# Kernel optimization log

Measured on AMD Instinct MI355X. Metric: run time of the kernel, lower is better.

## Reference

```python
import jax, jax.numpy as jnp
import numpy as np

N_HEADS = 8
N_GROUPS = 8  # n_channels=256 > 64
COLOR_WEIGHT = 1.2
EPS = 1e-5


def setup_inputs() -> dict:
    key = jax.random.key(0)
    ks = jax.random.split(key, 6)
    B, C, H, W = 16, 256, 32, 32
    x = jax.random.normal(ks[0], (B, C, H, W), dtype=jnp.float32)
    std = 0.02
    wq = jax.random.normal(ks[1], (C, C), dtype=jnp.float32) * std
    wk = jax.random.normal(ks[2], (C, C), dtype=jnp.float32) * std
    wv = jax.random.normal(ks[3], (C, C), dtype=jnp.float32) * std
    wo = jax.random.normal(ks[4], (C, C), dtype=jnp.float32) * std
    bq = jnp.zeros((C,), jnp.float32)
    bk = jnp.zeros((C,), jnp.float32)
    bv = jnp.zeros((C,), jnp.float32)
    bo = jnp.zeros((C,), jnp.float32)
    gn_w = jnp.ones((C,), jnp.float32)
    gn_b = jnp.zeros((C,), jnp.float32)
    return {"x": x, "wq": wq, "bq": bq, "wk": wk, "bk": bk,
            "wv": wv, "bv": bv, "wo": wo, "bo": bo,
            "gn_w": gn_w, "gn_b": gn_b}


def reference(x, wq, bq, wk, bk, wv, bv, wo, bo, gn_w, gn_b):
    B, C, H, W = x.shape
    S = H * W
    nh = N_HEADS
    hd = C // nh
    scale = hd ** (-0.5)

    # GroupNorm over (channels_per_group, spatial) per sample
    xf = x.reshape(B, C, S)
    xg = xf.reshape(B, N_GROUPS, (C // N_GROUPS) * S)
    mean = xg.mean(axis=-1, keepdims=True)
    var = xg.var(axis=-1, keepdims=True)
    xn = ((xg - mean) * jax.lax.rsqrt(var + EPS)).reshape(B, C, S)
    xn = xn * gn_w[None, :, None] + gn_b[None, :, None]

    xt = jnp.swapaxes(xn, 1, 2)  # [B, S, C]
    q = xt @ wq.T + bq
    k = xt @ wk.T + bk
    v = xt @ wv.T + bv
    # [B, S, C] -> [B, nh, S, hd]
    q = q.reshape(B, S, nh, hd).transpose(0, 2, 1, 3)
    k = k.reshape(B, S, nh, hd).transpose(0, 2, 1, 3)
    v = v.reshape(B, S, nh, hd).transpose(0, 2, 1, 3)

    attn = jnp.einsum('bhid,bhjd->bhij', q, k) * scale  # [B, nh, S, S]
    # color bias (is_grayscale=False path): k.transpose(-2,-1).reshape(B,nh,S,hd)
    k_color = jnp.swapaxes(k, -2, -1).reshape(B, nh, S, hd)
    color_attn = jnp.abs(q - k_color).mean(axis=-1, keepdims=True)  # [B,nh,S,1]
    attn = attn + COLOR_WEIGHT * color_attn
    attn = jax.nn.softmax(attn, axis=-1)
    # dropout is inference no-op

    out = jnp.einsum('bhij,bhjd->bhid', attn, v)  # [B, nh, S, hd]
    out = out.transpose(0, 2, 1, 3).reshape(B, S, C)
    out = out @ wo.T + bo
    out = jnp.swapaxes(out, 1, 2).reshape(B, C, H, W)
    return out
```

## Files before the change

kernel.cpp:

```cpp
#include <hip/hip_runtime.h>


typedef __attribute__((ext_vector_type(8))) short bf16x8;
typedef __attribute__((ext_vector_type(4))) float f32x4;

static __device__ __forceinline__ unsigned cvt_pk(float lo, float hi) {
  unsigned r;
  asm("v_cvt_pk_bf16_f32 %0, %1, %2" : "=v"(r) : "v"(lo), "v"(hi));
  return r;
}

__global__ __launch_bounds__(256) void gn_stats(
    const float* __restrict__ x, float2* __restrict__ stats) {
  __shared__ float red[8];
  int bg = blockIdx.x;
  const float4* x4 = (const float4*)(x + (size_t)bg * 32 * 1024);
  int tid = threadIdx.x;
  float s = 0.f, ss = 0.f;
  for (int i = tid; i < 8192; i += 256) {
    float4 vv = x4[i];
    s += (vv.x + vv.y) + (vv.z + vv.w);
    ss += vv.x * vv.x + vv.y * vv.y + vv.z * vv.z + vv.w * vv.w;
  }
#pragma unroll
  for (int o = 32; o > 0; o >>= 1) {
    s += __shfl_down(s, o);
    ss += __shfl_down(ss, o);
  }
  if ((tid & 63) == 0) { red[tid >> 6] = s; red[4 + (tid >> 6)] = ss; }
  __syncthreads();
  if (tid == 0) {
    float S = (red[0] + red[1]) + (red[2] + red[3]);
    float SS = (red[4] + red[5]) + (red[6] + red[7]);
    float mean = S * (1.f / 32768.f);
    float var = SS * (1.f / 32768.f) - mean * mean;
    stats[bg] = make_float2(mean, rsqrtf(var + 1e-5f));
  }
}

__global__ __launch_bounds__(256) void wconv(
    const float* __restrict__ w0, const float* __restrict__ w1,
    const float* __restrict__ w2, const float* __restrict__ w3,
    short* __restrict__ o0, short* __restrict__ o1,
    short* __restrict__ o2, short* __restrict__ o3) {
  int sel = blockIdx.y;
  const float* src = sel == 0 ? w0 : sel == 1 ? w1 : sel == 2 ? w2 : w3;
  short* dst = sel == 0 ? o0 : sel == 1 ? o1 : sel == 2 ? o2 : o3;
  int i = (blockIdx.x * 256 + threadIdx.x) * 8;
  float4 a = *(const float4*)(src + i);
  float4 b = *(const float4*)(src + i + 4);
  uint4 r;
  r.x = cvt_pk(a.x, a.y);
  r.y = cvt_pk(a.z, a.w);
  r.z = cvt_pk(b.x, b.y);
  r.w = cvt_pk(b.z, b.w);
  *(uint4*)(dst + i) = r;
}

__global__ __launch_bounds__(256, 4) void qkv_mfma(
    const float* __restrict__ x, const float2* __restrict__ stats,
    const float* __restrict__ gnw, const float* __restrict__ gnb,
    const short* __restrict__ Wq, const short* __restrict__ Wk,
    const short* __restrict__ Wv,
    const float* __restrict__ bq, const float* __restrict__ bk,
    const float* __restrict__ bv, short* __restrict__ outq,
    short* __restrict__ outk, short* __restrict__ outvt, float scaleq) {
  __shared__ __align__(16) char smem[20480];
  short* As = (short*)smem;
  int tid = threadIdx.x;
  int m0 = blockIdx.x * 64, n0 = blockIdx.y * 64;
  int w = tid >> 6, lane = tid & 63, g = lane >> 4, c = lane & 15;
  int wm = w >> 1, wn = w & 1;
  int srow = tid >> 2, sk = (tid & 3) * 8;
  int bsmp = m0 >> 10, s0 = m0 & 1023;
  int c2 = tid & 15, sg = tid >> 4;
  const float4* xb = (const float4*)(x + (size_t)(bsmp * 256) * 1024);
  unsigned* A32 = (unsigned*)As;
  f32x4 accq[2][2], acck[2][2], accv[2][2];
#pragma unroll
  for (int i = 0; i < 2; ++i)
#pragma unroll
    for (int j = 0; j < 2; ++j) {
      accq[i][j] = (f32x4){0.f, 0.f, 0.f, 0.f};
      acck[i][j] = (f32x4){0.f, 0.f, 0.f, 0.f};
      accv[i][j] = (f32x4){0.f, 0.f, 0.f, 0.f};
    }
  for (int kb = 0; kb < 8; ++kb) {
    float2 st = stats[bsmp * 8 + kb];
    int ch0 = kb * 32 + c2 * 2;
    float a0 = gnw[ch0] * st.y, b0v = gnb[ch0] - st.x * a0;
    float a1 = gnw[ch0 + 1] * st.y, b1v = gnb[ch0 + 1] - st.x * a1;
    float4 u = xb[(size_t)ch0 * 256 + (s0 >> 2) + sg];
    float4 v = xb[(size_t)(ch0 + 1) * 256 + (s0 >> 2) + sg];
    __syncthreads();
    {
      int r0 = (sg * 4) * 20 + c2;
      A32[r0]      = cvt_pk(u.x * a0 + b0v, v.x * a1 + b1v);
      A32[r0 + 20] = cvt_pk(u.y * a0 + b0v, v.y * a1 + b1v);
      A32[r0 + 40] = cvt_pk(u.z * a0 + b0v, v.z * a1 + b1v);
      A32[r0 + 60] = cvt_pk(u.w * a0 + b0v, v.w * a1 + b1v);
    }
    *(bf16x8*)(As + 2560 + srow * 40 + sk) =
        *(const bf16x8*)(Wq + (size_t)(n0 + srow) * 256 + kb * 32 + sk);
    *(bf16x8*)(As + 5120 + srow * 40 + sk) =
        *(const bf16x8*)(Wk + (size_t)(n0 + srow) * 256 + kb * 32 + sk);
    *(bf16x8*)(As + 7680 + srow * 40 + sk) =
        *(const bf16x8*)(Wv + (size_t)(n0 + srow) * 256 + kb * 32 + sk);
    __syncthreads();
    bf16x8 af[2], wfq[2], wfk[2], wfv[2];
#pragma unroll
    for (int i = 0; i < 2; ++i)
      af[i] = *(const bf16x8*)(As + (wm * 32 + i * 16 + c) * 40 + g * 8);
#pragma unroll
    for (int j = 0; j < 2; ++j) {
      int rr = (wn * 32 + j * 16 + c) * 40 + g * 8;
      wfq[j] = *(const bf16x8*)(As + 2560 + rr);
      wfk[j] = *(const bf16x8*)(As + 5120 + rr);
      wfv[j] = *(const bf16x8*)(As + 7680 + rr);
    }
#pragma unroll
    for (int i = 0; i < 2; ++i)
#pragma unroll
      for (int j = 0; j < 2; ++j) {
        accq[i][j] = __builtin_amdgcn_mfma_f32_16x16x32_bf16(wfq[j], af[i], accq[i][j], 0, 0, 0);
        acck[i][j] = __builtin_amdgcn_mfma_f32_16x16x32_bf16(wfk[j], af[i], acck[i][j], 0, 0, 0);
        accv[i][j] = __builtin_amdgcn_mfma_f32_16x16x32_bf16(af[i], wfv[j], accv[i][j], 0, 0, 0);
      }
  }
  __syncthreads();
  short* Tb = (short*)smem;
  int mrd = tid >> 2, ncol = (tid & 3) * 16;
#pragma unroll
  for (int i = 0; i < 2; ++i)
#pragma unroll
    for (int j = 0; j < 2; ++j) {
      float4 b4 = *(const float4*)&bq[n0 + wn * 32 + j * 16 + 4 * g];
      float v0 = (accq[i][j][0] + b4.x) * scaleq;
      float v1 = (accq[i][j][1] + b4.y) * scaleq;
      float v2 = (accq[i][j][2] + b4.z) * scaleq;
      float v3 = (accq[i][j][3] + b4.w) * scaleq;
      *(uint2*)(Tb + (wm * 32 + i * 16 + c) * 72 + wn * 32 + j * 16 + 4 * g) =
          make_uint2(cvt_pk(v0, v1), cvt_pk(v2, v3));
    }
  __syncthreads();
  {
    bf16x8 r0 = *(const bf16x8*)(Tb + mrd * 72 + ncol);
    bf16x8 r1 = *(const bf16x8*)(Tb + mrd * 72 + ncol + 8);
    short* dst = outq + (size_t)(m0 + mrd) * 256 + n0 + ncol;
    *(bf16x8*)dst = r0;
    *(bf16x8*)(dst + 8) = r1;
  }
  __syncthreads();
#pragma unroll
  for (int i = 0; i < 2; ++i)
#pragma unroll
    for (int j = 0; j < 2; ++j) {
      float4 b4 = *(const float4*)&bk[n0 + wn * 32 + j * 16 + 4 * g];
      float v0 = acck[i][j][0] + b4.x;
      float v1 = acck[i][j][1] + b4.y;
      float v2 = acck[i][j][2] + b4.z;
      float v3 = acck[i][j][3] + b4.w;
      *(uint2*)(Tb + (wm * 32 + i * 16 + c) * 72 + wn * 32 + j * 16 + 4 * g) =
          make_uint2(cvt_pk(v0, v1), cvt_pk(v2, v3));
    }
  __syncthreads();
  {
    bf16x8 r0 = *(const bf16x8*)(Tb + mrd * 72 + ncol);
    bf16x8 r1 = *(const bf16x8*)(Tb + mrd * 72 + ncol + 8);
    short* dst = outk + (size_t)(m0 + mrd) * 256 + n0 + ncol;
    *(bf16x8*)dst = r0;
    *(bf16x8*)(dst + 8) = r1;
  }
  __syncthreads();
#pragma unroll
  for (int i = 0; i < 2; ++i)
#pragma unroll
    for (int j = 0; j < 2; ++j) {
      float bvv = bv[n0 + wn * 32 + j * 16 + c];
      float v0 = accv[i][j][0] + bvv;
      float v1 = accv[i][j][1] + bvv;
      float v2 = accv[i][j][2] + bvv;
      float v3 = accv[i][j][3] + bvv;
      *(uint2*)(Tb + (wn * 32 + j * 16 + c) * 72 + wm * 32 + i * 16 + 4 * g) =
          make_uint2(cvt_pk(v0, v1), cvt_pk(v2, v3));
    }
  __syncthreads();
  {
    bf16x8 r0 = *(const bf16x8*)(Tb + mrd * 72 + ncol);
    bf16x8 r1 = *(const bf16x8*)(Tb + mrd * 72 + ncol + 8);
    short* dst = outvt + (size_t)(bsmp * 256 + n0 + mrd) * 1024 + s0 + ncol;
    *(bf16x8*)dst = r0;
    *(bf16x8*)(dst + 8) = r1;
  }
}

#define KSTR 40
#define VSTR 72
#define PSTR 72

__global__ __launch_bounds__(256, 4) void flash_mfma(
    const short* __restrict__ q, const short* __restrict__ k,
    const short* __restrict__ vt, short* __restrict__ out) {
  __shared__ short Ks[2][64 * KSTR];
  __shared__ short Vts[2][32 * VSTR];
  __shared__ short Ps[4 * 32 * PSTR];
  int bh = blockIdx.x, qt = blockIdx.y;
  int b = bh >> 3, h = bh & 7;
  int tid = threadIdx.x;
  int w = tid >> 6, lane = tid & 63, g = lane >> 4, c = lane & 15;
  short* Psw = Ps + w * 32 * PSTR;
  const size_t qrow0 = (size_t)b * 1024 + qt * 128 + w * 32;
  const int hoff = h * 32;
  bf16x8 aq[2];
#pragma unroll
  for (int mt = 0; mt < 2; ++mt)
    aq[mt] = *(const bf16x8*)(q + (qrow0 + mt * 16 + c) * 256 + hoff + g * 8);
  bf16x8 ones;
#pragma unroll
  for (int i = 0; i < 8; ++i) ones[i] = (short)0x3F80;
  f32x4 o_acc[2][2], accl[2];
#pragma unroll
  for (int mt = 0; mt < 2; ++mt) {
    accl[mt] = (f32x4){0.f, 0.f, 0.f, 0.f};
#pragma unroll
    for (int nt = 0; nt < 2; ++nt) o_acc[mt][nt] = (f32x4){0.f, 0.f, 0.f, 0.f};
  }
  const int kr = tid >> 2, kch = (tid & 3) * 8;
  const int vr = tid >> 3, vch = (tid & 7) * 8;
  const short* kbase = k + ((size_t)b * 1024) * 256 + hoff;
  const short* vbase = vt + (((size_t)b * 8 + h) * 32) * 1024;
  {
    bf16x8 k0 = *(const bf16x8*)(kbase + (size_t)kr * 256 + kch);
    bf16x8 v0 = *(const bf16x8*)(vbase + (size_t)vr * 1024 + vch);
    *(bf16x8*)(&Ks[0][kr * KSTR + kch]) = k0;
    *(bf16x8*)(&Vts[0][vr * VSTR + vch]) = v0;
  }
  __syncthreads();
  int cur = 0;
#pragma unroll 2
  for (int t = 0; t < 16; ++t) {
    bf16x8 kN, vN;
    if (t < 15) {
      kN = *(const bf16x8*)(kbase + (size_t)((t + 1) * 64 + kr) * 256 + kch);
      vN = *(const bf16x8*)(vbase + (size_t)vr * 1024 + (t + 1) * 64 + vch);
    }
    bf16x8 bk4[4];
#pragma unroll
    for (int kt = 0; kt < 4; ++kt)
      bk4[kt] = *(const bf16x8*)(&Ks[cur][(kt * 16 + c) * KSTR + g * 8]);
    f32x4 sc[2][4];
#pragma unroll
    for (int mt = 0; mt < 2; ++mt)
#pragma unroll
      for (int kt = 0; kt < 4; ++kt)
        sc[mt][kt] = __builtin_amdgcn_mfma_f32_16x16x32_bf16(
            bk4[kt], aq[mt], (f32x4){0.f, 0.f, 0.f, 0.f}, 0, 0, 0);
#pragma unroll
    for (int mt = 0; mt < 2; ++mt)
#pragma unroll
      for (int kt = 0; kt < 4; ++kt) {
        float p0 = __builtin_amdgcn_exp2f(sc[mt][kt][0]);
        float p1 = __builtin_amdgcn_exp2f(sc[mt][kt][1]);
        float p2 = __builtin_amdgcn_exp2f(sc[mt][kt][2]);
        float p3 = __builtin_amdgcn_exp2f(sc[mt][kt][3]);
        *(uint2*)(Psw + (mt * 16 + c) * PSTR + kt * 16 + 4 * g) =
            make_uint2(cvt_pk(p0, p1), cvt_pk(p2, p3));
      }
#pragma unroll
    for (int jt = 0; jt < 2; ++jt) {
      bf16x8 av[2], bp[2];
#pragma unroll
      for (int nt = 0; nt < 2; ++nt)
        av[nt] = *(const bf16x8*)(&Vts[cur][(nt * 16 + c) * VSTR + jt * 32 + g * 8]);
#pragma unroll
      for (int mt = 0; mt < 2; ++mt)
        bp[mt] = *(const bf16x8*)(Psw + (mt * 16 + c) * PSTR + jt * 32 + g * 8);
#pragma unroll
      for (int mt = 0; mt < 2; ++mt) {
#pragma unroll
        for (int nt = 0; nt < 2; ++nt)
          o_acc[mt][nt] = __builtin_amdgcn_mfma_f32_16x16x32_bf16(
              av[nt], bp[mt], o_acc[mt][nt], 0, 0, 0);
        accl[mt] = __builtin_amdgcn_mfma_f32_16x16x32_bf16(ones, bp[mt], accl[mt], 0, 0, 0);
      }
    }
    if (t < 15) {
      *(bf16x8*)(&Ks[cur ^ 1][kr * KSTR + kch]) = kN;
      *(bf16x8*)(&Vts[cur ^ 1][vr * VSTR + vch]) = vN;
      __syncthreads();
      cur ^= 1;
    }
  }
#pragma unroll
  for (int mt = 0; mt < 2; ++mt) {
    float linv = 1.0f / accl[mt][0];
#pragma unroll
    for (int nt = 0; nt < 2; ++nt) {
      float v0 = o_acc[mt][nt][0] * linv;
      float v1 = o_acc[mt][nt][1] * linv;
      float v2 = o_acc[mt][nt][2] * linv;
      float v3 = o_acc[mt][nt][3] * linv;
      *(uint2*)(out + (qrow0 + mt * 16 + c) * 256 + hoff + nt * 16 + 4 * g) =
          make_uint2(cvt_pk(v0, v1), cvt_pk(v2, v3));
    }
  }
}

__global__ __launch_bounds__(256) void gemm_out(
    const short* __restrict__ A, const short* __restrict__ W,
    const float* __restrict__ bias, float* __restrict__ out) {
  __shared__ __align__(16) char smem[10240];
  short* As = (short*)smem;
  short* Ws = (short*)(smem + 5120);
  int tid = threadIdx.x;
  int m0 = blockIdx.y * 64, n0 = blockIdx.x * 64;
  int w = tid >> 6, lane = tid & 63, g = lane >> 4, c = lane & 15;
  int wm = w >> 1, wn = w & 1;
  int srow = tid >> 2, sk = (tid & 3) * 8;
  f32x4 acc[2][2];
#pragma unroll
  for (int i = 0; i < 2; ++i)
#pragma unroll
    for (int j = 0; j < 2; ++j) acc[i][j] = (f32x4){0.f, 0.f, 0.f, 0.f};
  for (int kb = 0; kb < 8; ++kb) {
    __syncthreads();
    *(bf16x8*)(As + srow * 40 + sk) =
        *(const bf16x8*)(A + (size_t)(m0 + srow) * 256 + kb * 32 + sk);
    *(bf16x8*)(Ws + srow * 40 + sk) =
        *(const bf16x8*)(W + (size_t)(n0 + srow) * 256 + kb * 32 + sk);
    __syncthreads();
    bf16x8 af[2], wf[2];
#pragma unroll
    for (int i = 0; i < 2; ++i)
      af[i] = *(const bf16x8*)(As + (wm * 32 + i * 16 + c) * 40 + g * 8);
#pragma unroll
    for (int j = 0; j < 2; ++j)
      wf[j] = *(const bf16x8*)(Ws + (wn * 32 + j * 16 + c) * 40 + g * 8);
#pragma unroll
    for (int i = 0; i < 2; ++i)
#pragma unroll
      for (int j = 0; j < 2; ++j)
        acc[i][j] = __builtin_amdgcn_mfma_f32_16x16x32_bf16(af[i], wf[j], acc[i][j], 0, 0, 0);
  }
  int bsmp = m0 >> 10, s0 = m0 & 1023;
  float* Tf = (float*)smem;
  for (int half = 0; half < 2; ++half) {
    __syncthreads();
    if (wn == half) {
#pragma unroll
      for (int j = 0; j < 2; ++j) {
        float bvh = bias[n0 + half * 32 + j * 16 + c];
        int nl = j * 16 + c;
#pragma unroll
        for (int i = 0; i < 2; ++i)
#pragma unroll
          for (int r = 0; r < 4; ++r)
            Tf[nl * 68 + ((wm * 32 + i * 16 + 4 * g + r) ^ ((nl & 7) << 2))] =
                acc[i][j][r] + bvh;
      }
    }
    __syncthreads();
    int n = tid >> 3, mc = (tid & 7) * 8;
    float4 v0 = *(const float4*)(Tf + n * 68 + ((mc + 0) ^ ((n & 7) << 2)));
    float4 v1 = *(const float4*)(Tf + n * 68 + ((mc + 4) ^ ((n & 7) << 2)));
    float* dst = out + ((size_t)(bsmp * 256) + n0 + half * 32 + n) * 1024 + s0 + mc;
    *(float4*)dst = v0;
    *(float4*)(dst + 4) = v1;
  }
}

extern "C" void kernel_launch(void* const* d_in, const int* in_sizes, int n_in,
                              void* d_out, int out_size, void* d_ws, size_t ws_size,
                              hipStream_t stream) {
  const float* x   = (const float*)d_in[0];
  const float* wq  = (const float*)d_in[1];
  const float* bq  = (const float*)d_in[2];
  const float* wk  = (const float*)d_in[3];
  const float* bk  = (const float*)d_in[4];
  const float* wv  = (const float*)d_in[5];
  const float* bv  = (const float*)d_in[6];
  const float* wo  = (const float*)d_in[7];
  const float* bo  = (const float*)d_in[8];
  const float* gnw = (const float*)d_in[9];
  const float* gnb = (const float*)d_in[10];
  float* out = (float*)d_out;

  const size_t NE = (size_t)16 * 1024 * 256;
  short* sw  = (short*)d_ws;
  float2* stats = (float2*)sw;
  short* qb  = sw + NE;
  short* kb  = sw + 2 * NE;
  short* vtb = sw + 3 * NE;
  short* ao  = sw + 4 * NE;
  short* wqb = sw + 5 * NE;
  short* wkb = wqb + 65536;
  short* wvb = wkb + 65536;
  short* wob = wvb + 65536;

  const float SCALE_Q = (float)(0.17677669529663689 * 1.4426950408889634);
  dim3 blk(256);
  wconv<<<dim3(32, 4), blk, 0, stream>>>(wq, wk, wv, wo, wqb, wkb, wvb, wob);
  gn_stats<<<dim3(128), blk, 0, stream>>>(x, stats);
  qkv_mfma<<<dim3(256, 4), blk, 0, stream>>>(x, stats, gnw, gnb, wqb, wkb, wvb,
                                             bq, bk, bv, qb, kb, vtb, SCALE_Q);
  flash_mfma<<<dim3(128, 8), blk, 0, stream>>>(qb, kb, vtb, ao);
  gemm_out<<<dim3(4, 256), blk, 0, stream>>>(ao, wob, bo, out);
}
```

Baseline: 83.08 us.

## Double flash-attention block to 8 waves sharing each K/V tile load

```diff
diff --git a/kernel.cpp b/kernel.cpp
--- a/kernel.cpp
+++ b/kernel.cpp
@@ -198,18 +198,18 @@
 #define VSTR 72
 #define PSTR 72
 
-__global__ __launch_bounds__(256, 4) void flash_mfma(
+__global__ __launch_bounds__(512, 4) void flash_mfma(
     const short* __restrict__ q, const short* __restrict__ k,
     const short* __restrict__ vt, short* __restrict__ out) {
   __shared__ short Ks[2][64 * KSTR];
   __shared__ short Vts[2][32 * VSTR];
-  __shared__ short Ps[4 * 32 * PSTR];
+  __shared__ short Ps[8 * 32 * PSTR];
   int bh = blockIdx.x, qt = blockIdx.y;
   int b = bh >> 3, h = bh & 7;
   int tid = threadIdx.x;
   int w = tid >> 6, lane = tid & 63, g = lane >> 4, c = lane & 15;
   short* Psw = Ps + w * 32 * PSTR;
-  const size_t qrow0 = (size_t)b * 1024 + qt * 128 + w * 32;
+  const size_t qrow0 = (size_t)b * 1024 + qt * 256 + w * 32;
   const int hoff = h * 32;
   bf16x8 aq[2];
 #pragma unroll
@@ -225,24 +225,28 @@
 #pragma unroll
     for (int nt = 0; nt < 2; ++nt) o_acc[mt][nt] = (f32x4){0.f, 0.f, 0.f, 0.f};
   }
-  const int kr = tid >> 2, kch = (tid & 3) * 8;
-  const int vr = tid >> 3, vch = (tid & 7) * 8;
+  const bool doK = (tid < 256);
+  const int kr = (tid & 255) >> 2, kch = (tid & 3) * 8;
+  const int vr = (tid & 255) >> 3, vch = (tid & 7) * 8;
   const short* kbase = k + ((size_t)b * 1024) * 256 + hoff;
   const short* vbase = vt + (((size_t)b * 8 + h) * 32) * 1024;
-  {
-    bf16x8 k0 = *(const bf16x8*)(kbase + (size_t)kr * 256 + kch);
-    bf16x8 v0 = *(const bf16x8*)(vbase + (size_t)vr * 1024 + vch);
-    *(bf16x8*)(&Ks[0][kr * KSTR + kch]) = k0;
-    *(bf16x8*)(&Vts[0][vr * VSTR + vch]) = v0;
+  if (doK) {
+    *(bf16x8*)(&Ks[0][kr * KSTR + kch]) =
+        *(const bf16x8*)(kbase + (size_t)kr * 256 + kch);
+  } else {
+    *(bf16x8*)(&Vts[0][vr * VSTR + vch]) =
+        *(const bf16x8*)(vbase + (size_t)vr * 1024 + vch);
   }
   __syncthreads();
   int cur = 0;
 #pragma unroll 2
   for (int t = 0; t < 16; ++t) {
-    bf16x8 kN, vN;
+    bf16x8 nxt;
     if (t < 15) {
-      kN = *(const bf16x8*)(kbase + (size_t)((t + 1) * 64 + kr) * 256 + kch);
-      vN = *(const bf16x8*)(vbase + (size_t)vr * 1024 + (t + 1) * 64 + vch);
+      if (doK)
+        nxt = *(const bf16x8*)(kbase + (size_t)((t + 1) * 64 + kr) * 256 + kch);
+      else
+        nxt = *(const bf16x8*)(vbase + (size_t)vr * 1024 + (t + 1) * 64 + vch);
     }
     bf16x8 bk4[4];
 #pragma unroll
@@ -285,8 +289,10 @@
       }
     }
     if (t < 15) {
-      *(bf16x8*)(&Ks[cur ^ 1][kr * KSTR + kch]) = kN;
-      *(bf16x8*)(&Vts[cur ^ 1][vr * VSTR + vch]) = vN;
+      if (doK)
+        *(bf16x8*)(&Ks[cur ^ 1][kr * KSTR + kch]) = nxt;
+      else
+        *(bf16x8*)(&Vts[cur ^ 1][vr * VSTR + vch]) = nxt;
       __syncthreads();
       cur ^= 1;
     }
@@ -403,6 +409,6 @@
   gn_stats<<<dim3(128), blk, 0, stream>>>(x, stats);
   qkv_mfma<<<dim3(256, 4), blk, 0, stream>>>(x, stats, gnw, gnb, wqb, wkb, wvb,
                                              bq, bk, bv, qb, kb, vtb, SCALE_Q);
-  flash_mfma<<<dim3(128, 8), blk, 0, stream>>>(qb, kb, vtb, ao);
+  flash_mfma<<<dim3(128, 4), dim3(512), 0, stream>>>(qb, kb, vtb, ao);
   gemm_out<<<dim3(4, 256), blk, 0, stream>>>(ao, wob, bo, out);
 }
```

After: 84.94 us. +2.2%, slower.
